# Performance work log

Measured on AMD Instinct MI355X. Metric: run time of the kernel, lower is better.

## Reference

```python
import jax, jax.numpy as jnp
import numpy as np

C = 256
NUM_HEADS = 8
HEAD_DIM = C // NUM_HEADS
EPS = 1e-5


def setup_inputs() -> dict:
    key = jax.random.key(0)
    ks = jax.random.split(key, 12)
    b, h, w = 8, 64, 64
    s = 1.0 / np.sqrt(C)
    return {
        "cortical": jax.random.normal(ks[0], (b, C, h, w), jnp.float32),
        "subcortical": jax.random.normal(ks[1], (b, C, h, w), jnp.float32),
        "ventricular": jax.random.normal(ks[2], (b, C, h, w), jnp.float32),
        "in_proj_w": jax.random.uniform(ks[3], (3 * C, C), jnp.float32, -s, s),
        "in_proj_b": jnp.zeros((3 * C,), jnp.float32),
        "out_proj_w": jax.random.uniform(ks[4], (C, C), jnp.float32, -s, s),
        "out_proj_b": jnp.zeros((C,), jnp.float32),
        "ln_gamma": jnp.ones((C,), jnp.float32),
        "ln_beta": jnp.zeros((C,), jnp.float32),
        "conv_w": jax.random.uniform(ks[5], (C, 3 * C), jnp.float32, -1.0 / np.sqrt(3 * C), 1.0 / np.sqrt(3 * C)),
        "conv_b": jnp.zeros((C,), jnp.float32),
    }


def _forward(cortical, subcortical, ventricular,
             in_proj_w, in_proj_b, out_proj_w, out_proj_b,
             ln_gamma, ln_beta, conv_w, conv_b):
    b, c, h, w = cortical.shape
    # stack regions -> tokens of seq_len 3: (b,h,w,3,c) -> (N,3,c)
    regions = jnp.stack([cortical, subcortical, ventricular], axis=1)  # (b,3,c,h,w)
    x = regions.transpose(0, 3, 4, 1, 2).reshape(b * h * w, 3, c)
    # fused QKV projection
    qkv = x @ in_proj_w.T + in_proj_b  # (N,3,3c)
    q, k, v = jnp.split(qkv, 3, axis=-1)
    # split heads: (N,3,H,D)
    def heads(t):
        return t.reshape(-1, 3, NUM_HEADS, HEAD_DIM)
    q, k, v = heads(q), heads(k), heads(v)
    scores = jnp.einsum("nshd,nthd->nhst", q, k) / np.sqrt(HEAD_DIM)
    attn = jax.nn.softmax(scores, axis=-1)
    o = jnp.einsum("nhst,nthd->nshd", attn, v).reshape(-1, 3, c)
    o = o @ out_proj_w.T + out_proj_b
    # residual + LayerNorm over channels
    y = o + x
    mu = y.mean(-1, keepdims=True)
    var = y.var(-1, keepdims=True)
    y = (y - mu) * jax.lax.rsqrt(var + EPS) * ln_gamma + ln_beta
    # (N,3,c) -> (b,h,w,3c) region-major == torch cat along channel dim
    fused = y.reshape(b, h, w, 3 * c)
    out = fused @ conv_w.T + conv_b  # 1x1 conv as matmul
    return out.transpose(0, 3, 1, 2)  # (b,c,h,w)


def reference(cortical, subcortical, ventricular, in_proj_w, in_proj_b,
              out_proj_w, out_proj_b, ln_gamma, ln_beta, conv_w, conv_b):
    return _forward(cortical, subcortical, ventricular, in_proj_w, in_proj_b,
                    out_proj_w, out_proj_b, ln_gamma, ln_beta, conv_w, conv_b)
```

## Files before the change

kernel.cpp:

```cpp
#include <hip/hip_runtime.h>

typedef __bf16 bf16x8 __attribute__((ext_vector_type(8)));
typedef float  f32x4  __attribute__((ext_vector_type(4)));

#define XOFF 0
#define OOFF 49152
#define OBSZ 6144
#define PSOFF 73728
#define PQOFF 75264
#define MUOFF 76800
#define RSOFF 77184
#define SMEM_BYTES 77568
#define OB(g,b) (smem + OOFF + ((g) * 2 + (b)) * OBSZ)

__global__ void convert_weights(const float* __restrict__ w_in,
                                const float* __restrict__ w_out,
                                const float* __restrict__ w_conv,
                                __bf16* __restrict__ ws) {
  int gid = blockIdx.x * 256 + threadIdx.x;
  int i4 = gid * 4;
  const float* src;
  int off;
  if (i4 < 196608)      { src = w_in;   off = i4; }
  else if (i4 < 262144) { src = w_out;  off = i4 - 196608; }
  else                  { src = w_conv; off = i4 - 262144; }
  float4 f = *(const float4*)(src + off);
  ws[i4 + 0] = (__bf16)f.x;
  ws[i4 + 1] = (__bf16)f.y;
  ws[i4 + 2] = (__bf16)f.z;
  ws[i4 + 3] = (__bf16)f.w;
}

__global__ __launch_bounds__(256, 2) void crf_fused(
    const float* __restrict__ cort,
    const float* __restrict__ subc,
    const float* __restrict__ vent,
    const __bf16* __restrict__ w_in,
    const float* __restrict__ b_in,
    const __bf16* __restrict__ w_out,
    const float* __restrict__ b_out,
    const float* __restrict__ gamma,
    const float* __restrict__ beta,
    const __bf16* __restrict__ w_conv,
    const float* __restrict__ b_conv,
    float* __restrict__ out) {
  extern __shared__ char smem[];
  const int tid  = threadIdx.x;
  const int lane = tid & 63;
  const int wv   = tid >> 6;
  const int l15  = lane & 15;
  const int l4   = lane >> 4;
  const int blk  = blockIdx.x;
  const int img  = blk >> 7;
  const int pixbase = (blk & 127) << 5;
  const size_t base = (size_t)img * (256 * 4096) + pixbase;

  {
    const float* rp0 = cort + base;
    const float* rp1 = subc + base;
    const float* rp2 = vent + base;
#pragma unroll
    for (int si = 0; si < 3; ++si) {
      const float* rp = (si == 0) ? rp0 : (si == 1) ? rp1 : rp2;
#pragma unroll
      for (int t = 0; t < 8; ++t) {
        int idx = t * 256 + tid;
        int p4  = (idx & 7) * 4;
        int c   = idx >> 3;
        float4 f = *(const float4*)(rp + (size_t)c * 4096 + p4);
#pragma unroll
        for (int k = 0; k < 4; ++k) {
          int m = si * 32 + p4 + k;
          unsigned off = ((unsigned)(m * 512 + c * 2)) ^ ((unsigned)(m & 7) << 4);
          float fv = (k == 0) ? f.x : (k == 1) ? f.y : (k == 2) ? f.z : f.w;
          *(__bf16*)(smem + XOFF + off) = (__bf16)fv;
        }
      }
    }
  }

  f32x4 accY[6][4] = {};

  __syncthreads();

  const int ph = wv & 1;
  const int hg = wv >> 1;
  const float SC = 0.17677669529663687f;

  for (int hh = 0; hh < 4; ++hh) {
    const int h = hg * 4 + hh;
    float bq0 = b_in[h * 32 + l15],       bq1 = b_in[h * 32 + 16 + l15];
    float bk0 = b_in[256 + h * 32 + l15], bk1 = b_in[256 + h * 32 + 16 + l15];
    float bv0 = b_in[512 + h * 32 + l15], bv1 = b_in[512 + h * 32 + 16 + l15];

    f32x4 acc[3][6] = {};
    bf16x8 bb[2][6];
#pragma unroll
    for (int j = 0; j < 6; ++j) {
      int jb = (j >> 1) * 256 + h * 32 + (j & 1) * 16 + l15;
      bb[0][j] = *(const bf16x8*)(w_in + (size_t)jb * 256 + l4 * 8);
    }
#pragma unroll
    for (int ks = 0; ks < 8; ++ks) {
      const int k0 = ks * 32;
      if (ks < 7) {
#pragma unroll
        for (int j = 0; j < 6; ++j) {
          int jb = (j >> 1) * 256 + h * 32 + (j & 1) * 16 + l15;
          bb[(ks + 1) & 1][j] = *(const bf16x8*)(w_in + (size_t)jb * 256 + k0 + 32 + l4 * 8);
        }
      }
      bf16x8 af[3];
#pragma unroll
      for (int s = 0; s < 3; ++s) {
        int m = s * 32 + ph * 16 + l15;
        unsigned off = ((unsigned)(m * 512 + (k0 + l4 * 8) * 2)) ^ ((unsigned)(m & 7) << 4);
        af[s] = *(const bf16x8*)(smem + XOFF + off);
      }
#pragma unroll
      for (int s = 0; s < 3; ++s)
#pragma unroll
        for (int j = 0; j < 6; ++j)
          acc[s][j] = __builtin_amdgcn_mfma_f32_16x16x32_bf16(af[s], bb[ks & 1][j], acc[s][j], 0, 0, 0);
    }
#pragma unroll
    for (int s = 0; s < 3; ++s)
#pragma unroll
      for (int r = 0; r < 4; ++r) {
        acc[s][0][r] += bq0; acc[s][1][r] += bq1;
        acc[s][2][r] += bk0; acc[s][3][r] += bk1;
        acc[s][4][r] += bv0; acc[s][5][r] += bv1;
      }

    char* ob = OB(hg, hh & 1);
#pragma unroll
    for (int si = 0; si < 3; ++si) {
      float pp[3][4];
#pragma unroll
      for (int ti = 0; ti < 3; ++ti)
#pragma unroll
        for (int r = 0; r < 4; ++r)
          pp[ti][r] = acc[si][0][r] * acc[ti][2][r] + acc[si][1][r] * acc[ti][3][r];
#pragma unroll
      for (int mask = 1; mask <= 8; mask <<= 1)
#pragma unroll
        for (int ti = 0; ti < 3; ++ti)
#pragma unroll
          for (int r = 0; r < 4; ++r)
            pp[ti][r] += __shfl_xor(pp[ti][r], mask);
#pragma unroll
      for (int r = 0; r < 4; ++r) {
        float s0 = pp[0][r] * SC, s1 = pp[1][r] * SC, s2 = pp[2][r] * SC;
        float mx = fmaxf(fmaxf(s0, s1), s2);
        float e0 = __expf(s0 - mx), e1 = __expf(s1 - mx), e2 = __expf(s2 - mx);
        float inv = 1.f / (e0 + e1 + e2);
        e0 *= inv; e1 *= inv; e2 *= inv;
        int m = si * 32 + ph * 16 + l4 * 4 + r;
#pragma unroll
        for (int jq = 0; jq < 2; ++jq) {
          float ov = e0 * acc[0][4 + jq][r] + e1 * acc[1][4 + jq][r] + e2 * acc[2][4 + jq][r];
          unsigned off = ((unsigned)(m * 64 + (jq * 16 + l15) * 2)) ^ ((unsigned)(m & 7) << 4);
          *(__bf16*)(ob + off) = (__bf16)ov;
        }
      }
    }
    __syncthreads();

    {
      const int b = hh & 1;
      bf16x8 afA[6], afB[6], bfA[4], bfB[4];
#pragma unroll
      for (int i = 0; i < 6; ++i) {
        int row = i * 16 + l15;
        unsigned off = ((unsigned)(row * 64 + l4 * 16)) ^ ((unsigned)(row & 7) << 4);
        afA[i] = *(const bf16x8*)(OB(0, b) + off);
        afB[i] = *(const bf16x8*)(OB(1, b) + off);
      }
#pragma unroll
      for (int j = 0; j < 4; ++j) {
        int jr = wv * 64 + j * 16 + l15;
        bfA[j] = *(const bf16x8*)(w_out + (size_t)jr * 256 + hh * 32 + l4 * 8);
        bfB[j] = *(const bf16x8*)(w_out + (size_t)jr * 256 + (4 + hh) * 32 + l4 * 8);
      }
#pragma unroll
      for (int i = 0; i < 6; ++i)
#pragma unroll
        for (int j = 0; j < 4; ++j) {
          accY[i][j] = __builtin_amdgcn_mfma_f32_16x16x32_bf16(afA[i], bfA[j], accY[i][j], 0, 0, 0);
          accY[i][j] = __builtin_amdgcn_mfma_f32_16x16x32_bf16(afB[i], bfB[j], accY[i][j], 0, 0, 0);
        }
    }
  }

  float bo[4], gg[4], bb2[4];
#pragma unroll
  for (int j = 0; j < 4; ++j) {
    int jc = wv * 64 + j * 16 + l15;
    bo[j] = b_out[jc];
    gg[j] = gamma[jc];
    bb2[j] = beta[jc];
  }
#pragma unroll
  for (int i = 0; i < 6; ++i)
#pragma unroll
    for (int r = 0; r < 4; ++r) {
      int m = i * 16 + l4 * 4 + r;
      float s1 = 0.f, s2 = 0.f;
#pragma unroll
      for (int j = 0; j < 4; ++j) {
        int jc = wv * 64 + j * 16 + l15;
        unsigned xo = ((unsigned)(m * 512 + jc * 2)) ^ ((unsigned)(m & 7) << 4);
        float xv = (float)(*(const __bf16*)(smem + XOFF + xo));
        float v = accY[i][j][r] + bo[j] + xv;
        accY[i][j][r] = v;
        s1 += v;
        s2 += v * v;
      }
      s1 += __shfl_xor(s1, 1); s2 += __shfl_xor(s2, 1);
      s1 += __shfl_xor(s1, 2); s2 += __shfl_xor(s2, 2);
      s1 += __shfl_xor(s1, 4); s2 += __shfl_xor(s2, 4);
      s1 += __shfl_xor(s1, 8); s2 += __shfl_xor(s2, 8);
      if (l15 == 0) {
        *(float*)(smem + PSOFF + (m * 4 + wv) * 4) = s1;
        *(float*)(smem + PQOFF + (m * 4 + wv) * 4) = s2;
      }
    }
  __syncthreads();
  if (tid < 96) {
    float s = 0.f, q = 0.f;
#pragma unroll
    for (int j = 0; j < 4; ++j) {
      s += *(const float*)(smem + PSOFF + (tid * 4 + j) * 4);
      q += *(const float*)(smem + PQOFF + (tid * 4 + j) * 4);
    }
    float mu  = s * (1.f / 256.f);
    float var = q * (1.f / 256.f) - mu * mu;
    *(float*)(smem + MUOFF + tid * 4) = mu;
    *(float*)(smem + RSOFF + tid * 4) = rsqrtf(var + 1e-5f);
  }
  __syncthreads();
#pragma unroll
  for (int i = 0; i < 6; ++i)
#pragma unroll
    for (int r = 0; r < 4; ++r) {
      int m = i * 16 + l4 * 4 + r;
      float mu = *(const float*)(smem + MUOFF + m * 4);
      float rs = *(const float*)(smem + RSOFF + m * 4);
      int s = m >> 5, p = m & 31;
#pragma unroll
      for (int j = 0; j < 4; ++j) {
        int jc = wv * 64 + j * 16 + l15;
        float yv = (accY[i][j][r] - mu) * rs * gg[j] + bb2[j];
        int kk = s * 256 + jc;
        unsigned off = ((unsigned)(p * 1536 + kk * 2)) ^ ((unsigned)(p & 7) << 4);
        *(__bf16*)(smem + XOFF + off) = (__bf16)yv;
      }
    }
  __syncthreads();

  {
    f32x4 accC[4][2] = {};
#pragma unroll 4
    for (int ks = 0; ks < 24; ++ks) {
      const int k0 = ks * 32;
      bf16x8 af[4], bfr2[2];
#pragma unroll
      for (int i = 0; i < 4; ++i) {
        int co = wv * 64 + i * 16 + l15;
        af[i] = *(const bf16x8*)(w_conv + (size_t)co * 768 + k0 + l4 * 8);
      }
#pragma unroll
      for (int j = 0; j < 2; ++j) {
        int p = j * 16 + l15;
        unsigned off = ((unsigned)(p * 1536 + (k0 + l4 * 8) * 2)) ^ ((unsigned)(p & 7) << 4);
        bfr2[j] = *(const bf16x8*)(smem + XOFF + off);
      }
#pragma unroll
      for (int i = 0; i < 4; ++i)
#pragma unroll
        for (int j = 0; j < 2; ++j)
          accC[i][j] = __builtin_amdgcn_mfma_f32_16x16x32_bf16(af[i], bfr2[j], accC[i][j], 0, 0, 0);
    }
#pragma unroll
    for (int i = 0; i < 4; ++i)
#pragma unroll
      for (int r = 0; r < 4; ++r) {
        int co = wv * 64 + i * 16 + l4 * 4 + r;
        float cb = b_conv[co];
#pragma unroll
        for (int j = 0; j < 2; ++j)
          out[((size_t)img * 256 + co) * 4096 + pixbase + j * 16 + l15] = accC[i][j][r] + cb;
      }
  }
}

extern "C" void kernel_launch(void* const* d_in, const int* in_sizes, int n_in,
                              void* d_out, int out_size, void* d_ws, size_t ws_size,
                              hipStream_t stream) {
  (void)in_sizes; (void)n_in; (void)out_size; (void)ws_size;
  const float* cort    = (const float*)d_in[0];
  const float* subc    = (const float*)d_in[1];
  const float* vent    = (const float*)d_in[2];
  const float* w_in_f  = (const float*)d_in[3];
  const float* b_in    = (const float*)d_in[4];
  const float* w_out_f = (const float*)d_in[5];
  const float* b_out   = (const float*)d_in[6];
  const float* gamma   = (const float*)d_in[7];
  const float* beta    = (const float*)d_in[8];
  const float* w_conv_f= (const float*)d_in[9];
  const float* b_conv  = (const float*)d_in[10];

  __bf16* ws = (__bf16*)d_ws;
  convert_weights<<<448, 256, 0, stream>>>(w_in_f, w_out_f, w_conv_f, ws);
  crf_fused<<<1024, 256, SMEM_BYTES, stream>>>(
      cort, subc, vent,
      ws,            b_in,
      ws + 196608,   b_out,
      gamma,         beta,
      ws + 262144,   b_conv,
      (float*)d_out);
}
```

Baseline: 240.1 us.

## Widen LDS XOR swizzle, pad attention-output buffers, pack bf16 pair stores

The LDS swizzle for the staged input and LayerNorm tiles now XORs with row&31 instead of row&7, and the per-head attention-output buffers switch from swizzled 64-byte rows to padded 80-byte rows. Together these are meant to cut LDS bank conflicts. The input staging loop loads two channels per thread and writes them as one packed 32-bit bf16 pair instead of two scalar stores. The in_proj weight register double-buffering is dropped in favour of plain per-step loads. To make room, the partial-sum buffers now alias the output-buffer region, which needs an extra barrier and slightly more LDS, and removing the prefetch may expose global load latency.

```diff
diff --git a/kernel.cpp b/kernel.cpp
--- a/kernel.cpp
+++ b/kernel.cpp
@@ -5,13 +5,18 @@
 
 #define XOFF 0
 #define OOFF 49152
-#define OBSZ 6144
-#define PSOFF 73728
-#define PQOFF 75264
-#define MUOFF 76800
-#define RSOFF 77184
-#define SMEM_BYTES 77568
-#define OB(g,b) (smem + OOFF + ((g) * 2 + (b)) * OBSZ)
+#define OBUFSZ 7680
+#define PSOFF 49152
+#define PQOFF 50688
+#define MUOFF 52224
+#define RSOFF 52608
+#define SMEM_BYTES 79872
+#define OB(g,b) (smem + OOFF + ((g) * 2 + (b)) * OBUFSZ)
+
+static __device__ __forceinline__ unsigned short f2b(float f) {
+  __bf16 h = (__bf16)f;
+  return __builtin_bit_cast(unsigned short, h);
+}
 
 __global__ void convert_weights(const float* __restrict__ w_in,
                                 const float* __restrict__ w_out,
@@ -56,24 +61,23 @@
   const size_t base = (size_t)img * (256 * 4096) + pixbase;
 
   {
-    const float* rp0 = cort + base;
-    const float* rp1 = subc + base;
-    const float* rp2 = vent + base;
+    const int p4 = (tid & 7) * 4;
 #pragma unroll
     for (int si = 0; si < 3; ++si) {
-      const float* rp = (si == 0) ? rp0 : (si == 1) ? rp1 : rp2;
-#pragma unroll
-      for (int t = 0; t < 8; ++t) {
-        int idx = t * 256 + tid;
-        int p4  = (idx & 7) * 4;
-        int c   = idx >> 3;
-        float4 f = *(const float4*)(rp + (size_t)c * 4096 + p4);
+      const float* rp = (si == 0) ? cort : (si == 1) ? subc : vent;
+      rp += base;
+#pragma unroll
+      for (int t = 0; t < 4; ++t) {
+        int c = t * 64 + (tid >> 3) * 2;
+        float4 fa = *(const float4*)(rp + (size_t)c * 4096 + p4);
+        float4 fb = *(const float4*)(rp + (size_t)(c + 1) * 4096 + p4);
 #pragma unroll
         for (int k = 0; k < 4; ++k) {
           int m = si * 32 + p4 + k;
-          unsigned off = ((unsigned)(m * 512 + c * 2)) ^ ((unsigned)(m & 7) << 4);
-          float fv = (k == 0) ? f.x : (k == 1) ? f.y : (k == 2) ? f.z : f.w;
-          *(__bf16*)(smem + XOFF + off) = (__bf16)fv;
+          float va = (k == 0) ? fa.x : (k == 1) ? fa.y : (k == 2) ? fa.z : fa.w;
+          float vb = (k == 0) ? fb.x : (k == 1) ? fb.y : (k == 2) ? fb.z : fb.w;
+          unsigned off = ((unsigned)(m * 512 + c * 2)) ^ ((unsigned)(m & 31) << 4);
+          *(unsigned*)(smem + XOFF + off) = (unsigned)f2b(va) | ((unsigned)f2b(vb) << 16);
         }
       }
     }
@@ -94,34 +98,26 @@
     float bv0 = b_in[512 + h * 32 + l15], bv1 = b_in[512 + h * 32 + 16 + l15];
 
     f32x4 acc[3][6] = {};
-    bf16x8 bb[2][6];
-#pragma unroll
-    for (int j = 0; j < 6; ++j) {
-      int jb = (j >> 1) * 256 + h * 32 + (j & 1) * 16 + l15;
-      bb[0][j] = *(const bf16x8*)(w_in + (size_t)jb * 256 + l4 * 8);
-    }
 #pragma unroll
     for (int ks = 0; ks < 8; ++ks) {
       const int k0 = ks * 32;
-      if (ks < 7) {
-#pragma unroll
-        for (int j = 0; j < 6; ++j) {
-          int jb = (j >> 1) * 256 + h * 32 + (j & 1) * 16 + l15;
-          bb[(ks + 1) & 1][j] = *(const bf16x8*)(w_in + (size_t)jb * 256 + k0 + 32 + l4 * 8);
-        }
-      }
-      bf16x8 af[3];
+      bf16x8 af[3], bfr[6];
 #pragma unroll
       for (int s = 0; s < 3; ++s) {
         int m = s * 32 + ph * 16 + l15;
-        unsigned off = ((unsigned)(m * 512 + (k0 + l4 * 8) * 2)) ^ ((unsigned)(m & 7) << 4);
+        unsigned off = ((unsigned)(m * 512 + (k0 + l4 * 8) * 2)) ^ ((unsigned)(m & 31) << 4);
         af[s] = *(const bf16x8*)(smem + XOFF + off);
       }
 #pragma unroll
+      for (int j = 0; j < 6; ++j) {
+        int jb = (j >> 1) * 256 + h * 32 + (j & 1) * 16 + l15;
+        bfr[j] = *(const bf16x8*)(w_in + (size_t)jb * 256 + k0 + l4 * 8);
+      }
+#pragma unroll
       for (int s = 0; s < 3; ++s)
 #pragma unroll
         for (int j = 0; j < 6; ++j)
-          acc[s][j] = __builtin_amdgcn_mfma_f32_16x16x32_bf16(af[s], bb[ks & 1][j], acc[s][j], 0, 0, 0);
+          acc[s][j] = __builtin_amdgcn_mfma_f32_16x16x32_bf16(af[s], bfr[j], acc[s][j], 0, 0, 0);
     }
 #pragma unroll
     for (int s = 0; s < 3; ++s)
@@ -159,8 +155,7 @@
 #pragma unroll
         for (int jq = 0; jq < 2; ++jq) {
           float ov = e0 * acc[0][4 + jq][r] + e1 * acc[1][4 + jq][r] + e2 * acc[2][4 + jq][r];
-          unsigned off = ((unsigned)(m * 64 + (jq * 16 + l15) * 2)) ^ ((unsigned)(m & 7) << 4);
-          *(__bf16*)(ob + off) = (__bf16)ov;
+          *(__bf16*)(ob + m * 80 + (jq * 16 + l15) * 2) = (__bf16)ov;
         }
       }
     }
@@ -171,10 +166,9 @@
       bf16x8 afA[6], afB[6], bfA[4], bfB[4];
 #pragma unroll
       for (int i = 0; i < 6; ++i) {
-        int row = i * 16 + l15;
-        unsigned off = ((unsigned)(row * 64 + l4 * 16)) ^ ((unsigned)(row & 7) << 4);
-        afA[i] = *(const bf16x8*)(OB(0, b) + off);
-        afB[i] = *(const bf16x8*)(OB(1, b) + off);
+        int ro = (i * 16 + l15) * 80 + l4 * 16;
+        afA[i] = *(const bf16x8*)(OB(0, b) + ro);
+        afB[i] = *(const bf16x8*)(OB(1, b) + ro);
       }
 #pragma unroll
       for (int j = 0; j < 4; ++j) {
@@ -191,6 +185,7 @@
         }
     }
   }
+  __syncthreads();
 
   float bo[4], gg[4], bb2[4];
 #pragma unroll
@@ -209,7 +204,7 @@
 #pragma unroll
       for (int j = 0; j < 4; ++j) {
         int jc = wv * 64 + j * 16 + l15;
-        unsigned xo = ((unsigned)(m * 512 + jc * 2)) ^ ((unsigned)(m & 7) << 4);
+        unsigned xo = ((unsigned)(m * 512 + jc * 2)) ^ ((unsigned)(m & 31) << 4);
         float xv = (float)(*(const __bf16*)(smem + XOFF + xo));
         float v = accY[i][j][r] + bo[j] + xv;
         accY[i][j][r] = v;
@@ -252,7 +247,7 @@
         int jc = wv * 64 + j * 16 + l15;
         float yv = (accY[i][j][r] - mu) * rs * gg[j] + bb2[j];
         int kk = s * 256 + jc;
-        unsigned off = ((unsigned)(p * 1536 + kk * 2)) ^ ((unsigned)(p & 7) << 4);
+        unsigned off = ((unsigned)(p * 1536 + kk * 2)) ^ ((unsigned)(p & 31) << 4);
         *(__bf16*)(smem + XOFF + off) = (__bf16)yv;
       }
     }
@@ -272,7 +267,7 @@
 #pragma unroll
       for (int j = 0; j < 2; ++j) {
         int p = j * 16 + l15;
-        unsigned off = ((unsigned)(p * 1536 + (k0 + l4 * 8) * 2)) ^ ((unsigned)(p & 7) << 4);
+        unsigned off = ((unsigned)(p * 1536 + (k0 + l4 * 8) * 2)) ^ ((unsigned)(p & 31) << 4);
         bfr2[j] = *(const bf16x8*)(smem + XOFF + off);
       }
 #pragma unroll
```

Result: faster. 200.5 us (-16.5%).
